# Performance work log

Measured on AMD Instinct MI355X. Metric: run time of the kernel, lower is better.

## Reference

```python
import jax, jax.numpy as jnp
import numpy as np

N_USERS = 100000
N_ITEMS = 50000
DIM = 64
N_EDGES = 4_000_000
NUM_LAYERS = 3


def setup_inputs() -> dict:
    key = jax.random.key(0)
    k1, k2, k3 = jax.random.split(key, 3)
    # xavier_uniform-like scale for embeddings
    scale = float(np.sqrt(6.0 / (N_USERS + DIM)))
    user_emb = jax.random.uniform(k1, (N_USERS, DIM), jnp.float32, -scale, scale)
    scale_i = float(np.sqrt(6.0 / (N_ITEMS + DIM)))
    item_emb = jax.random.uniform(k2, (N_ITEMS, DIM), jnp.float32, -scale_i, scale_i)
    edge_index = jax.random.randint(k3, (2, N_EDGES), 0, N_USERS + N_ITEMS, dtype=jnp.int64)
    return {"user_emb": user_emb, "item_emb": item_emb, "edge_index": edge_index}


def reference(user_emb, item_emb, edge_index):
    """LightGCN_W.encode_window: K rounds of symmetric-normalized SpMM, then layer mean."""
    n_users = user_emb.shape[0]
    n_nodes = n_users + item_emb.shape[0]
    row, col = edge_index[0], edge_index[1]  # messages flow row (source) -> col (target)

    # gcn_norm with add_self_loops=False (PyG LGConv default)
    ones = jnp.ones(row.shape[0], dtype=user_emb.dtype)
    deg = jax.ops.segment_sum(ones, col, num_segments=n_nodes)
    dinv = jnp.where(deg > 0, jax.lax.rsqrt(jnp.maximum(deg, 1e-12)), 0.0)
    norm = (dinv[row] * dinv[col])[:, None]  # [E, 1]

    x = jnp.concatenate([user_emb, item_emb], axis=0)  # [N, D]
    acc = x
    for _ in range(NUM_LAYERS):
        x = jax.ops.segment_sum(norm * x[row], col, num_segments=n_nodes)
        acc = acc + x
    out = acc / (NUM_LAYERS + 1)
    return out[:n_users], out[n_users:]
```

## Files before the change

### kernel.cpp

```cpp
#include <hip/hip_runtime.h>
#include <hip/hip_fp16.h>

#define DIM 64
#define BSH 8
#define BMASK 255u
#define NBMAX 1024
#define BINC 16384


__global__ void zero_ints(int* __restrict__ p, int n) {
    int i = blockIdx.x * blockDim.x + threadIdx.x;
    if (i < n) p[i] = 0;
}

__global__ __launch_bounds__(1024) void bucket_count_kernel(const int* __restrict__ edge, int E,
                                                            int* __restrict__ bcnt, int NB) {
    __shared__ int lcnt[NBMAX];
    for (int i = threadIdx.x; i < NB; i += 1024) lcnt[i] = 0;
    __syncthreads();
    int stride = gridDim.x * 1024;
    for (int i = blockIdx.x * 1024 + threadIdx.x; i < E; i += stride)
        atomicAdd(&lcnt[edge[E + i] >> BSH], 1);
    __syncthreads();
    for (int i = threadIdx.x; i < NB; i += 1024) {
        int v = lcnt[i];
        if (v) atomicAdd(&bcnt[i], v);
    }
}

__global__ __launch_bounds__(1024) void scan_kernel(const int* __restrict__ cnt,
                                                    int* __restrict__ offsets,
                                                    int* __restrict__ cursor,
                                                    int n) {
    __shared__ int lds[1024];
    const int T = 1024, K = 4, CHUNK = T * K;
    int carry = 0;
    for (int base = 0; base < n; base += CHUNK) {
        int v[K];
        int idx0 = base + (int)threadIdx.x * K;
#pragma unroll
        for (int k = 0; k < K; ++k) {
            int i = idx0 + k;
            v[k] = (i < n) ? cnt[i] : 0;
        }
        int tsum = v[0] + v[1] + v[2] + v[3];
        lds[threadIdx.x] = tsum;
        __syncthreads();
        int incl = tsum;
        for (int off = 1; off < T; off <<= 1) {
            int t = (threadIdx.x >= (unsigned)off) ? lds[threadIdx.x - off] : 0;
            __syncthreads();
            incl += t;
            lds[threadIdx.x] = incl;
            __syncthreads();
        }
        int total = lds[T - 1];
        int run = carry + (incl - tsum);
#pragma unroll
        for (int k = 0; k < K; ++k) {
            int i = idx0 + k;
            if (i < n) { offsets[i] = run; cursor[i] = run; }
            run += v[k];
        }
        carry += total;
        __syncthreads();
    }
    if (threadIdx.x == 0) offsets[n] = carry;
}

__global__ __launch_bounds__(1024) void bin_kernel(const int* __restrict__ edge, int E,
                                                   int* __restrict__ bcur,
                                                   unsigned* __restrict__ bin, int NB) {
    __shared__ unsigned stage[BINC];
    __shared__ int lcnt[NBMAX];
    __shared__ int lsc[NBMAX];
    __shared__ int lcur[NBMAX];
    __shared__ int gb[NBMAX];
    const int tid = (int)threadIdx.x;
    const int beg = (int)blockIdx.x * BINC;
    const int n = min(BINC, E - beg);

    lcnt[tid] = 0;
    __syncthreads();
    for (int i = tid; i < n; i += 1024)
        atomicAdd(&lcnt[edge[E + beg + i] >> BSH], 1);
    __syncthreads();
    lsc[tid] = lcnt[tid];
    __syncthreads();
    for (int off = 1; off < 1024; off <<= 1) {
        int t = (tid >= off) ? lsc[tid - off] : 0;
        __syncthreads();
        lsc[tid] += t;
        __syncthreads();
    }
    {
        int cb = lcnt[tid];
        lcur[tid] = lsc[tid] - cb;
        if (tid < NB) gb[tid] = cb ? atomicAdd(&bcur[tid], cb) : 0;
    }
    __syncthreads();
    for (int i = tid; i < n; i += 1024) {
        int r = edge[beg + i];
        int c = edge[E + beg + i];
        int b = c >> BSH;
        int slot = atomicAdd(&lcur[b], 1);
        stage[slot] = ((unsigned)r << BSH) | ((unsigned)c & BMASK);
    }
    __syncthreads();
    const int wid = tid >> 6, lane = tid & 63;
    for (int b = wid; b < NB; b += 16) {
        int cb = lcnt[b];
        if (!cb) continue;
        int lb = lsc[b] - cb;
        int g = gb[b];
        for (int l = lane; l < cb; l += 64)
            bin[g + l] = stage[lb + l];
    }
}

__global__ __launch_bounds__(256) void csr_kernel(const unsigned* __restrict__ bin,
                                                  const int* __restrict__ boff,
                                                  const float* __restrict__ user,
                                                  const float* __restrict__ item,
                                                  int nU,
                                                  int* __restrict__ offsets,
                                                  float* __restrict__ dinv,
                                                  float* __restrict__ rdinv,
                                                  int* __restrict__ row_sorted,
                                                  __half* __restrict__ y0,
                                                  int nN) {
    __shared__ int lcnt[256];
    __shared__ int lsc[256];
    __shared__ int lcur[256];
    __shared__ float sdinv[256];
    const int tid = (int)threadIdx.x;
    const int b = (int)blockIdx.x;
    const int beg = boff[b], end = boff[b + 1];
    lcnt[tid] = 0;
    __syncthreads();
    for (int i = beg + tid; i < end; i += 256)
        atomicAdd(&lcnt[bin[i] & BMASK], 1);
    __syncthreads();
    lsc[tid] = lcnt[tid];
    __syncthreads();
    for (int off = 1; off < 256; off <<= 1) {
        int t = (tid >= off) ? lsc[tid - off] : 0;
        __syncthreads();
        lsc[tid] += t;
        __syncthreads();
    }
    int cb = lcnt[tid];
    int lb = lsc[tid] - cb;
    lcur[tid] = lb;
    float dv = cb ? rsqrtf((float)cb) : 0.0f;
    sdinv[tid] = dv;
    int node = (b << BSH) + tid;
    if (node < nN) {
        offsets[node] = beg + lb;
        dinv[node] = dv;
        rdinv[node] = cb ? sqrtf((float)cb) : 0.0f;
        if (node == nN - 1) offsets[nN] = beg + lsc[tid];
    }
    __syncthreads();
    for (int i = beg + tid; i < end; i += 256) {
        unsigned e = bin[i];
        int c = (int)(e & BMASK);
        int p = atomicAdd(&lcur[c], 1);
        row_sorted[beg + p] = (int)(e >> BSH);
    }
    const int baseNode = b << BSH;
#pragma unroll
    for (int it = 0; it < 8; ++it) {
        int idx = it * 256 + tid;
        int ln = idx >> 3;
        int node2 = baseNode + ln;
        if (node2 < nN) {
            int qc = idx & 7;
            const float* src = (node2 < nU) ? user + (size_t)node2 * DIM
                                            : item + (size_t)(node2 - nU) * DIM;
            float4 e0 = ((const float4*)src)[qc * 2];
            float4 e1 = ((const float4*)src)[qc * 2 + 1];
            float dvn = sdinv[ln];
            float4 pack;
            __half2* p = (__half2*)&pack;
            p[0] = __floats2half2_rn(dvn * e0.x, dvn * e0.y);
            p[1] = __floats2half2_rn(dvn * e0.z, dvn * e0.w);
            p[2] = __floats2half2_rn(dvn * e1.x, dvn * e1.y);
            p[3] = __floats2half2_rn(dvn * e1.z, dvn * e1.w);
            ((float4*)y0)[(size_t)baseNode * 8 + idx] = pack;
        }
    }
}

__global__ __launch_bounds__(256) void layer_kernel(const int* __restrict__ offsets,
                                                    const int* __restrict__ row_sorted,
                                                    const float* __restrict__ dinv,
                                                    const __half* __restrict__ y_in,
                                                    __half* __restrict__ y_out,
                                                    int nN) {
    int wave = (int)((blockIdx.x * blockDim.x + threadIdx.x) >> 6);
    int lane = (int)(threadIdx.x & 63);
    if (wave >= nN) return;
    const int beg = offsets[wave];
    const int end = offsets[wave + 1];
    const int g = lane >> 3;
    const int q = lane & 7;
    const float4* yv = (const float4*)y_in;
    float a0 = 0, a1 = 0, a2 = 0, a3 = 0, a4 = 0, a5 = 0, a6 = 0, a7 = 0;
    const int last = end - 1;
    for (int base = beg; base < end; base += 16) {
        int e0 = base + g;
        int e1 = e0 + 8;
        int i0 = (e0 <= last) ? e0 : last;
        int i1 = (e1 <= last) ? e1 : last;
        float m0 = (e0 <= last) ? 1.0f : 0.0f;
        float m1 = (e1 <= last) ? 1.0f : 0.0f;
        int r0 = row_sorted[i0];
        int r1 = row_sorted[i1];
        float4 v0 = yv[(size_t)r0 * 8 + q];
        float4 v1 = yv[(size_t)r1 * 8 + q];
        const __half2* h0 = (const __half2*)&v0;
        const __half2* h1 = (const __half2*)&v1;
        float2 t;
        t = __half22float2(h0[0]); a0 = fmaf(m0, t.x, a0); a1 = fmaf(m0, t.y, a1);
        t = __half22float2(h0[1]); a2 = fmaf(m0, t.x, a2); a3 = fmaf(m0, t.y, a3);
        t = __half22float2(h0[2]); a4 = fmaf(m0, t.x, a4); a5 = fmaf(m0, t.y, a5);
        t = __half22float2(h0[3]); a6 = fmaf(m0, t.x, a6); a7 = fmaf(m0, t.y, a7);
        t = __half22float2(h1[0]); a0 = fmaf(m1, t.x, a0); a1 = fmaf(m1, t.y, a1);
        t = __half22float2(h1[1]); a2 = fmaf(m1, t.x, a2); a3 = fmaf(m1, t.y, a3);
        t = __half22float2(h1[2]); a4 = fmaf(m1, t.x, a4); a5 = fmaf(m1, t.y, a5);
        t = __half22float2(h1[3]); a6 = fmaf(m1, t.x, a6); a7 = fmaf(m1, t.y, a7);
    }
#pragma unroll
    for (int ofs = 8; ofs <= 32; ofs <<= 1) {
        a0 += __shfl_xor(a0, ofs);
        a1 += __shfl_xor(a1, ofs);
        a2 += __shfl_xor(a2, ofs);
        a3 += __shfl_xor(a3, ofs);
        a4 += __shfl_xor(a4, ofs);
        a5 += __shfl_xor(a5, ofs);
        a6 += __shfl_xor(a6, ofs);
        a7 += __shfl_xor(a7, ofs);
    }
    if (g == 0) {
        float dc = dinv[wave];
        float s = dc * dc;
        float4 pack;
        __half2* p = (__half2*)&pack;
        p[0] = __floats2half2_rn(s * a0, s * a1);
        p[1] = __floats2half2_rn(s * a2, s * a3);
        p[2] = __floats2half2_rn(s * a4, s * a5);
        p[3] = __floats2half2_rn(s * a6, s * a7);
        ((float4*)y_out)[(size_t)wave * 8 + q] = pack;
    }
}

__global__ __launch_bounds__(256) void final_kernel(const float* __restrict__ user,
                                                    const float* __restrict__ item,
                                                    const float* __restrict__ rdinv,
                                                    const __half* __restrict__ y1,
                                                    const __half* __restrict__ y2,
                                                    const __half* __restrict__ y3,
                                                    float* __restrict__ out,
                                                    int nU, int nN) {
    int c = blockIdx.x * blockDim.x + threadIdx.x;
    if (c >= nN * 8) return;
    int node = c >> 3;
    int qc = c & 7;
    float rd = 0.25f * rdinv[node];
    float4 h1 = ((const float4*)y1)[c];
    float4 h2 = ((const float4*)y2)[c];
    float4 h3 = ((const float4*)y3)[c];
    const float* src = (node < nU) ? user + (size_t)node * DIM
                                   : item + (size_t)(node - nU) * DIM;
    float4 e0 = ((const float4*)src)[qc * 2];
    float4 e1 = ((const float4*)src)[qc * 2 + 1];
    const __half2* p1 = (const __half2*)&h1;
    const __half2* p2 = (const __half2*)&h2;
    const __half2* p3 = (const __half2*)&h3;
    float r[8];
#pragma unroll
    for (int j = 0; j < 4; ++j) {
        float2 u1 = __half22float2(p1[j]);
        float2 u2 = __half22float2(p2[j]);
        float2 u3 = __half22float2(p3[j]);
        r[2 * j]     = u1.x + u2.x + u3.x;
        r[2 * j + 1] = u1.y + u2.y + u3.y;
    }
    float4 o0, o1;
    o0.x = 0.25f * e0.x + rd * r[0];
    o0.y = 0.25f * e0.y + rd * r[1];
    o0.z = 0.25f * e0.z + rd * r[2];
    o0.w = 0.25f * e0.w + rd * r[3];
    o1.x = 0.25f * e1.x + rd * r[4];
    o1.y = 0.25f * e1.y + rd * r[5];
    o1.z = 0.25f * e1.z + rd * r[6];
    o1.w = 0.25f * e1.w + rd * r[7];
    ((float4*)out)[(size_t)c * 2]     = o0;
    ((float4*)out)[(size_t)c * 2 + 1] = o1;
}


extern "C" void kernel_launch(void* const* d_in, const int* in_sizes, int n_in,
                              void* d_out, int out_size, void* d_ws, size_t ws_size,
                              hipStream_t stream) {
    const float* user = (const float*)d_in[0];
    const float* item = (const float*)d_in[1];
    const int*   edge = (const int*)d_in[2];

    const int nU = in_sizes[0] / DIM;
    const int nI = in_sizes[1] / DIM;
    const int nN = nU + nI;
    const int E  = in_sizes[2] / 2;
    const int total = nN * DIM;
    const int NB = (nN + 255) / 256;

    float* out = (float*)d_out;

    char* ws = (char*)d_ws;
    size_t off = 0;
    auto take = [&](size_t bytes) -> char* {
        char* p = ws + off;
        off = (off + bytes + 255) & ~(size_t)255;
        return p;
    };
    const size_t ybytes = (size_t)total * 2;
    const size_t binbytes = (size_t)E * 4;
    int*      bcnt       = (int*)  take((size_t)NB * 4);
    int*      boff       = (int*)  take((size_t)(NB + 1) * 4);
    int*      bcur       = (int*)  take((size_t)NB * 4);
    int*      offsets    = (int*)  take((size_t)(nN + 1) * 4);
    float*    dinv       = (float*)take((size_t)nN * 4);
    float*    rdinv      = (float*)take((size_t)nN * 4);
    int*      row_sorted = (int*)  take((size_t)E * 4);
    char*     regionA    = take(binbytes > ybytes ? binbytes : ybytes);
    char*     regionB    = take(ybytes);
    char*     regionC    = take(ybytes);
    unsigned* bin = (unsigned*)regionA;
    __half*   y1  = (__half*)regionA;
    __half*   y0  = (__half*)regionB;
    __half*   y3  = (__half*)regionB;
    __half*   y2  = (__half*)regionC;
    (void)ws_size; (void)n_in; (void)out_size;

    const int B = 256;
    dim3 blk(B);

    zero_ints<<<dim3((NB + B - 1) / B), blk, 0, stream>>>(bcnt, NB);
    bucket_count_kernel<<<dim3(256), dim3(1024), 0, stream>>>(edge, E, bcnt, NB);
    scan_kernel<<<dim3(1), dim3(1024), 0, stream>>>(bcnt, boff, bcur, NB);
    bin_kernel<<<dim3((E + BINC - 1) / BINC), dim3(1024), 0, stream>>>(edge, E, bcur, bin, NB);
    csr_kernel<<<dim3(NB), blk, 0, stream>>>(bin, boff, user, item, nU,
                                             offsets, dinv, rdinv, row_sorted, y0, nN);

    dim3 lgrid((nN + 3) / 4);
    layer_kernel<<<lgrid, blk, 0, stream>>>(offsets, row_sorted, dinv, y0, y1, nN);
    layer_kernel<<<lgrid, blk, 0, stream>>>(offsets, row_sorted, dinv, y1, y2, nN);
    layer_kernel<<<lgrid, blk, 0, stream>>>(offsets, row_sorted, dinv, y2, y3, nN);

    final_kernel<<<dim3((nN * 8 + B - 1) / B), blk, 0, stream>>>(user, item, rdinv,
                                                                 y1, y2, y3, out, nU, nN);
}
```

Measured before the change: 319.2 us.

## Split fp16 feature matrix into two 32-column halves and run per-half layer passes

```diff
diff --git a/kernel.cpp b/kernel.cpp
--- a/kernel.cpp
+++ b/kernel.cpp
@@ -2,10 +2,13 @@
 #include <hip/hip_fp16.h>
 
 #define DIM 64
+#define HDIM 32
 #define BSH 8
 #define BMASK 255u
 #define NBMAX 1024
 #define BINC 16384
+
+typedef __attribute__((ext_vector_type(4))) float f32x4;
 
 
 __global__ void zero_ints(int* __restrict__ p, int n) {
@@ -127,7 +130,8 @@
                                                   float* __restrict__ dinv,
                                                   float* __restrict__ rdinv,
                                                   int* __restrict__ row_sorted,
-                                                  __half* __restrict__ y0,
+                                                  __half* __restrict__ y0A,
+                                                  __half* __restrict__ y0B,
                                                   int nN) {
     __shared__ int lcnt[256];
     __shared__ int lsc[256];
@@ -187,38 +191,41 @@
             p[1] = __floats2half2_rn(dvn * e0.z, dvn * e0.w);
             p[2] = __floats2half2_rn(dvn * e1.x, dvn * e1.y);
             p[3] = __floats2half2_rn(dvn * e1.z, dvn * e1.w);
-            ((float4*)y0)[(size_t)baseNode * 8 + idx] = pack;
+            float4* dst = (qc < 4)
+                ? (float4*)y0A + (size_t)node2 * 4 + qc
+                : (float4*)y0B + (size_t)node2 * 4 + (qc - 4);
+            *dst = pack;
         }
     }
 }
 
-__global__ __launch_bounds__(256) void layer_kernel(const int* __restrict__ offsets,
-                                                    const int* __restrict__ row_sorted,
-                                                    const float* __restrict__ dinv,
-                                                    const __half* __restrict__ y_in,
-                                                    __half* __restrict__ y_out,
-                                                    int nN) {
+__global__ __launch_bounds__(256) void layer_pass_kernel(const int* __restrict__ offsets,
+                                                         const int* __restrict__ row_sorted,
+                                                         const float* __restrict__ dinv,
+                                                         const __half* __restrict__ y_in,
+                                                         __half* __restrict__ y_out,
+                                                         int nN) {
     int wave = (int)((blockIdx.x * blockDim.x + threadIdx.x) >> 6);
     int lane = (int)(threadIdx.x & 63);
     if (wave >= nN) return;
     const int beg = offsets[wave];
     const int end = offsets[wave + 1];
-    const int g = lane >> 3;
-    const int q = lane & 7;
+    const int g = lane >> 2;
+    const int q = lane & 3;
     const float4* yv = (const float4*)y_in;
     float a0 = 0, a1 = 0, a2 = 0, a3 = 0, a4 = 0, a5 = 0, a6 = 0, a7 = 0;
     const int last = end - 1;
-    for (int base = beg; base < end; base += 16) {
+    for (int base = beg; base < end; base += 32) {
         int e0 = base + g;
-        int e1 = e0 + 8;
+        int e1 = e0 + 16;
         int i0 = (e0 <= last) ? e0 : last;
         int i1 = (e1 <= last) ? e1 : last;
         float m0 = (e0 <= last) ? 1.0f : 0.0f;
         float m1 = (e1 <= last) ? 1.0f : 0.0f;
-        int r0 = row_sorted[i0];
-        int r1 = row_sorted[i1];
-        float4 v0 = yv[(size_t)r0 * 8 + q];
-        float4 v1 = yv[(size_t)r1 * 8 + q];
+        int r0 = __builtin_nontemporal_load(row_sorted + i0);
+        int r1 = __builtin_nontemporal_load(row_sorted + i1);
+        float4 v0 = yv[(size_t)r0 * 4 + q];
+        float4 v1 = yv[(size_t)r1 * 4 + q];
         const __half2* h0 = (const __half2*)&v0;
         const __half2* h1 = (const __half2*)&v1;
         float2 t;
@@ -232,7 +239,7 @@
         t = __half22float2(h1[3]); a6 = fmaf(m1, t.x, a6); a7 = fmaf(m1, t.y, a7);
     }
 #pragma unroll
-    for (int ofs = 8; ofs <= 32; ofs <<= 1) {
+    for (int ofs = 4; ofs <= 32; ofs <<= 1) {
         a0 += __shfl_xor(a0, ofs);
         a1 += __shfl_xor(a1, ofs);
         a2 += __shfl_xor(a2, ofs);
@@ -245,22 +252,26 @@
     if (g == 0) {
         float dc = dinv[wave];
         float s = dc * dc;
-        float4 pack;
-        __half2* p = (__half2*)&pack;
-        p[0] = __floats2half2_rn(s * a0, s * a1);
-        p[1] = __floats2half2_rn(s * a2, s * a3);
-        p[2] = __floats2half2_rn(s * a4, s * a5);
-        p[3] = __floats2half2_rn(s * a6, s * a7);
-        ((float4*)y_out)[(size_t)wave * 8 + q] = pack;
+        f32x4 pack;
+        __half2 ph[4];
+        ph[0] = __floats2half2_rn(s * a0, s * a1);
+        ph[1] = __floats2half2_rn(s * a2, s * a3);
+        ph[2] = __floats2half2_rn(s * a4, s * a5);
+        ph[3] = __floats2half2_rn(s * a6, s * a7);
+        pack = *(const f32x4*)ph;
+        __builtin_nontemporal_store(pack, (f32x4*)y_out + (size_t)wave * 4 + q);
     }
 }
 
 __global__ __launch_bounds__(256) void final_kernel(const float* __restrict__ user,
                                                     const float* __restrict__ item,
                                                     const float* __restrict__ rdinv,
-                                                    const __half* __restrict__ y1,
-                                                    const __half* __restrict__ y2,
-                                                    const __half* __restrict__ y3,
+                                                    const __half* __restrict__ y1A,
+                                                    const __half* __restrict__ y1B,
+                                                    const __half* __restrict__ y2A,
+                                                    const __half* __restrict__ y2B,
+                                                    const __half* __restrict__ y3A,
+                                                    const __half* __restrict__ y3B,
                                                     float* __restrict__ out,
                                                     int nU, int nN) {
     int c = blockIdx.x * blockDim.x + threadIdx.x;
@@ -268,9 +279,13 @@
     int node = c >> 3;
     int qc = c & 7;
     float rd = 0.25f * rdinv[node];
-    float4 h1 = ((const float4*)y1)[c];
-    float4 h2 = ((const float4*)y2)[c];
-    float4 h3 = ((const float4*)y3)[c];
+    size_t hidx = (size_t)node * 4 + (qc & 3);
+    const __half* t1 = (qc < 4) ? y1A : y1B;
+    const __half* t2 = (qc < 4) ? y2A : y2B;
+    const __half* t3 = (qc < 4) ? y3A : y3B;
+    float4 h1 = ((const float4*)t1)[hidx];
+    float4 h2 = ((const float4*)t2)[hidx];
+    float4 h3 = ((const float4*)t3)[hidx];
     const float* src = (node < nU) ? user + (size_t)node * DIM
                                    : item + (size_t)(node - nU) * DIM;
     float4 e0 = ((const float4*)src)[qc * 2];
@@ -312,7 +327,6 @@
     const int nI = in_sizes[1] / DIM;
     const int nN = nU + nI;
     const int E  = in_sizes[2] / 2;
-    const int total = nN * DIM;
     const int NB = (nN + 255) / 256;
 
     float* out = (float*)d_out;
@@ -324,7 +338,7 @@
         off = (off + bytes + 255) & ~(size_t)255;
         return p;
     };
-    const size_t ybytes = (size_t)total * 2;
+    const size_t hbytes = (size_t)nN * HDIM * 2;
     const size_t binbytes = (size_t)E * 4;
     int*      bcnt       = (int*)  take((size_t)NB * 4);
     int*      boff       = (int*)  take((size_t)(NB + 1) * 4);
@@ -333,14 +347,18 @@
     float*    dinv       = (float*)take((size_t)nN * 4);
     float*    rdinv      = (float*)take((size_t)nN * 4);
     int*      row_sorted = (int*)  take((size_t)E * 4);
-    char*     regionA    = take(binbytes > ybytes ? binbytes : ybytes);
-    char*     regionB    = take(ybytes);
-    char*     regionC    = take(ybytes);
-    unsigned* bin = (unsigned*)regionA;
-    __half*   y1  = (__half*)regionA;
-    __half*   y0  = (__half*)regionB;
-    __half*   y3  = (__half*)regionB;
-    __half*   y2  = (__half*)regionC;
+    char*     R1 = take(binbytes > 2 * hbytes ? binbytes : 2 * hbytes);
+    char*     R2 = take(2 * hbytes);
+    char*     R3 = take(2 * hbytes);
+    unsigned* bin = (unsigned*)R1;
+    __half*   y1A = (__half*)R1;
+    __half*   y1B = (__half*)(R1 + hbytes);
+    __half*   y0A = (__half*)R2;
+    __half*   y0B = (__half*)(R2 + hbytes);
+    __half*   y3A = y0A;
+    __half*   y3B = y0B;
+    __half*   y2A = (__half*)R3;
+    __half*   y2B = (__half*)(R3 + hbytes);
     (void)ws_size; (void)n_in; (void)out_size;
 
     const int B = 256;
@@ -351,13 +369,17 @@
     scan_kernel<<<dim3(1), dim3(1024), 0, stream>>>(bcnt, boff, bcur, NB);
     bin_kernel<<<dim3((E + BINC - 1) / BINC), dim3(1024), 0, stream>>>(edge, E, bcur, bin, NB);
     csr_kernel<<<dim3(NB), blk, 0, stream>>>(bin, boff, user, item, nU,
-                                             offsets, dinv, rdinv, row_sorted, y0, nN);
+                                             offsets, dinv, rdinv, row_sorted, y0A, y0B, nN);
 
     dim3 lgrid((nN + 3) / 4);
-    layer_kernel<<<lgrid, blk, 0, stream>>>(offsets, row_sorted, dinv, y0, y1, nN);
-    layer_kernel<<<lgrid, blk, 0, stream>>>(offsets, row_sorted, dinv, y1, y2, nN);
-    layer_kernel<<<lgrid, blk, 0, stream>>>(offsets, row_sorted, dinv, y2, y3, nN);
+    layer_pass_kernel<<<lgrid, blk, 0, stream>>>(offsets, row_sorted, dinv, y0A, y1A, nN);
+    layer_pass_kernel<<<lgrid, blk, 0, stream>>>(offsets, row_sorted, dinv, y0B, y1B, nN);
+    layer_pass_kernel<<<lgrid, blk, 0, stream>>>(offsets, row_sorted, dinv, y1A, y2A, nN);
+    layer_pass_kernel<<<lgrid, blk, 0, stream>>>(offsets, row_sorted, dinv, y1B, y2B, nN);
+    layer_pass_kernel<<<lgrid, blk, 0, stream>>>(offsets, row_sorted, dinv, y2A, y3A, nN);
+    layer_pass_kernel<<<lgrid, blk, 0, stream>>>(offsets, row_sorted, dinv, y2B, y3B, nN);
 
     final_kernel<<<dim3((nN * 8 + B - 1) / B), blk, 0, stream>>>(user, item, rdinv,
-                                                                 y1, y2, y3, out, nU, nN);
-}
+                                                                 y1A, y1B, y2A, y2B, y3A, y3B,
+                                                                 out, nU, nN);
+}
```

Result: slower. 478.3 us (+49.8%).

## Pad CSR rows to multiples of 16 with sentinel zero row to drop masking

Applied to the files above, without the earlier changes.

```diff
diff --git a/kernel.cpp b/kernel.cpp
--- a/kernel.cpp
+++ b/kernel.cpp
@@ -6,6 +6,9 @@
 #define BMASK 255u
 #define NBMAX 1024
 #define BINC 16384
+#define PADSTRIDE 4096
+
+typedef __attribute__((ext_vector_type(4))) float f32x4;
 
 
 __global__ void zero_ints(int* __restrict__ p, int n) {
@@ -123,15 +126,17 @@
                                                   const float* __restrict__ user,
                                                   const float* __restrict__ item,
                                                   int nU,
-                                                  int* __restrict__ offsets,
+                                                  int* __restrict__ poff,
+                                                  int* __restrict__ pcnt,
                                                   float* __restrict__ dinv,
                                                   float* __restrict__ rdinv,
-                                                  int* __restrict__ row_sorted,
+                                                  int* __restrict__ row_padded,
                                                   __half* __restrict__ y0,
                                                   int nN) {
     __shared__ int lcnt[256];
-    __shared__ int lsc[256];
+    __shared__ int lps[256];
     __shared__ int lcur[256];
+    __shared__ int spbeg[256];
     __shared__ float sdinv[256];
     const int tid = (int)threadIdx.x;
     const int b = (int)blockIdx.x;
@@ -141,33 +146,38 @@
     for (int i = beg + tid; i < end; i += 256)
         atomicAdd(&lcnt[bin[i] & BMASK], 1);
     __syncthreads();
-    lsc[tid] = lcnt[tid];
+    const int cb = lcnt[tid];
+    const int pc = (cb + 15) & ~15;
+    lps[tid] = pc;
     __syncthreads();
     for (int off = 1; off < 256; off <<= 1) {
-        int t = (tid >= off) ? lsc[tid - off] : 0;
-        __syncthreads();
-        lsc[tid] += t;
-        __syncthreads();
-    }
-    int cb = lcnt[tid];
-    int lb = lsc[tid] - cb;
-    lcur[tid] = lb;
+        int t = (tid >= off) ? lps[tid - off] : 0;
+        __syncthreads();
+        lps[tid] += t;
+        __syncthreads();
+    }
+    const int pbase = beg + b * PADSTRIDE;
+    const int pbeg = pbase + (lps[tid] - pc);
+    spbeg[tid] = pbeg;
+    lcur[tid] = pbeg;
     float dv = cb ? rsqrtf((float)cb) : 0.0f;
     sdinv[tid] = dv;
     int node = (b << BSH) + tid;
     if (node < nN) {
-        offsets[node] = beg + lb;
+        poff[node] = pbeg;
+        pcnt[node] = pc;
         dinv[node] = dv;
         rdinv[node] = cb ? sqrtf((float)cb) : 0.0f;
-        if (node == nN - 1) offsets[nN] = beg + lsc[tid];
     }
     __syncthreads();
     for (int i = beg + tid; i < end; i += 256) {
         unsigned e = bin[i];
         int c = (int)(e & BMASK);
         int p = atomicAdd(&lcur[c], 1);
-        row_sorted[beg + p] = (int)(e >> BSH);
-    }
+        row_padded[p] = (int)(e >> BSH);
+    }
+    for (int k = cb; k < pc; ++k)
+        row_padded[spbeg[tid] + k] = nN;
     const int baseNode = b << BSH;
 #pragma unroll
     for (int it = 0; it < 8; ++it) {
@@ -192,44 +202,48 @@
     }
 }
 
-__global__ __launch_bounds__(256) void layer_kernel(const int* __restrict__ offsets,
-                                                    const int* __restrict__ row_sorted,
+__global__ void zero_row_kernel(__half* __restrict__ r1, __half* __restrict__ r2,
+                                __half* __restrict__ r3, int nN) {
+    int t = threadIdx.x;
+    size_t o = (size_t)nN * DIM + t;
+    r1[o] = __float2half(0.0f);
+    r2[o] = __float2half(0.0f);
+    r3[o] = __float2half(0.0f);
+}
+
+__global__ __launch_bounds__(256) void layer_kernel(const int* __restrict__ poff,
+                                                    const int* __restrict__ pcnt,
                                                     const float* __restrict__ dinv,
+                                                    const int* __restrict__ row_padded,
                                                     const __half* __restrict__ y_in,
                                                     __half* __restrict__ y_out,
                                                     int nN) {
     int wave = (int)((blockIdx.x * blockDim.x + threadIdx.x) >> 6);
     int lane = (int)(threadIdx.x & 63);
     if (wave >= nN) return;
-    const int beg = offsets[wave];
-    const int end = offsets[wave + 1];
+    const int beg = poff[wave];
+    const int n = pcnt[wave];
     const int g = lane >> 3;
     const int q = lane & 7;
     const float4* yv = (const float4*)y_in;
     float a0 = 0, a1 = 0, a2 = 0, a3 = 0, a4 = 0, a5 = 0, a6 = 0, a7 = 0;
-    const int last = end - 1;
-    for (int base = beg; base < end; base += 16) {
-        int e0 = base + g;
-        int e1 = e0 + 8;
-        int i0 = (e0 <= last) ? e0 : last;
-        int i1 = (e1 <= last) ? e1 : last;
-        float m0 = (e0 <= last) ? 1.0f : 0.0f;
-        float m1 = (e1 <= last) ? 1.0f : 0.0f;
-        int r0 = row_sorted[i0];
-        int r1 = row_sorted[i1];
+    for (int base = 0; base < n; base += 16) {
+        int e0 = beg + base + g;
+        int r0 = __builtin_nontemporal_load(row_padded + e0);
+        int r1 = __builtin_nontemporal_load(row_padded + e0 + 8);
         float4 v0 = yv[(size_t)r0 * 8 + q];
         float4 v1 = yv[(size_t)r1 * 8 + q];
         const __half2* h0 = (const __half2*)&v0;
         const __half2* h1 = (const __half2*)&v1;
         float2 t;
-        t = __half22float2(h0[0]); a0 = fmaf(m0, t.x, a0); a1 = fmaf(m0, t.y, a1);
-        t = __half22float2(h0[1]); a2 = fmaf(m0, t.x, a2); a3 = fmaf(m0, t.y, a3);
-        t = __half22float2(h0[2]); a4 = fmaf(m0, t.x, a4); a5 = fmaf(m0, t.y, a5);
-        t = __half22float2(h0[3]); a6 = fmaf(m0, t.x, a6); a7 = fmaf(m0, t.y, a7);
-        t = __half22float2(h1[0]); a0 = fmaf(m1, t.x, a0); a1 = fmaf(m1, t.y, a1);
-        t = __half22float2(h1[1]); a2 = fmaf(m1, t.x, a2); a3 = fmaf(m1, t.y, a3);
-        t = __half22float2(h1[2]); a4 = fmaf(m1, t.x, a4); a5 = fmaf(m1, t.y, a5);
-        t = __half22float2(h1[3]); a6 = fmaf(m1, t.x, a6); a7 = fmaf(m1, t.y, a7);
+        t = __half22float2(h0[0]); a0 += t.x; a1 += t.y;
+        t = __half22float2(h0[1]); a2 += t.x; a3 += t.y;
+        t = __half22float2(h0[2]); a4 += t.x; a5 += t.y;
+        t = __half22float2(h0[3]); a6 += t.x; a7 += t.y;
+        t = __half22float2(h1[0]); a0 += t.x; a1 += t.y;
+        t = __half22float2(h1[1]); a2 += t.x; a3 += t.y;
+        t = __half22float2(h1[2]); a4 += t.x; a5 += t.y;
+        t = __half22float2(h1[3]); a6 += t.x; a7 += t.y;
     }
 #pragma unroll
     for (int ofs = 8; ofs <= 32; ofs <<= 1) {
@@ -245,13 +259,13 @@
     if (g == 0) {
         float dc = dinv[wave];
         float s = dc * dc;
-        float4 pack;
-        __half2* p = (__half2*)&pack;
-        p[0] = __floats2half2_rn(s * a0, s * a1);
-        p[1] = __floats2half2_rn(s * a2, s * a3);
-        p[2] = __floats2half2_rn(s * a4, s * a5);
-        p[3] = __floats2half2_rn(s * a6, s * a7);
-        ((float4*)y_out)[(size_t)wave * 8 + q] = pack;
+        __half2 ph[4];
+        ph[0] = __floats2half2_rn(s * a0, s * a1);
+        ph[1] = __floats2half2_rn(s * a2, s * a3);
+        ph[2] = __floats2half2_rn(s * a4, s * a5);
+        ph[3] = __floats2half2_rn(s * a6, s * a7);
+        f32x4 pack = *(const f32x4*)ph;
+        __builtin_nontemporal_store(pack, (f32x4*)y_out + (size_t)wave * 8 + q);
     }
 }
 
@@ -312,7 +326,6 @@
     const int nI = in_sizes[1] / DIM;
     const int nN = nU + nI;
     const int E  = in_sizes[2] / 2;
-    const int total = nN * DIM;
     const int NB = (nN + 255) / 256;
 
     float* out = (float*)d_out;
@@ -324,23 +337,25 @@
         off = (off + bytes + 255) & ~(size_t)255;
         return p;
     };
-    const size_t ybytes = (size_t)total * 2;
+    const size_t ytab = (size_t)(nN + 1) * DIM * 2;
     const size_t binbytes = (size_t)E * 4;
+    const size_t padbytes = ((size_t)E + (size_t)NB * PADSTRIDE) * 4;
     int*      bcnt       = (int*)  take((size_t)NB * 4);
     int*      boff       = (int*)  take((size_t)(NB + 1) * 4);
     int*      bcur       = (int*)  take((size_t)NB * 4);
-    int*      offsets    = (int*)  take((size_t)(nN + 1) * 4);
+    int*      poff       = (int*)  take((size_t)nN * 4);
+    int*      pcnt       = (int*)  take((size_t)nN * 4);
     float*    dinv       = (float*)take((size_t)nN * 4);
     float*    rdinv      = (float*)take((size_t)nN * 4);
-    int*      row_sorted = (int*)  take((size_t)E * 4);
-    char*     regionA    = take(binbytes > ybytes ? binbytes : ybytes);
-    char*     regionB    = take(ybytes);
-    char*     regionC    = take(ybytes);
-    unsigned* bin = (unsigned*)regionA;
-    __half*   y1  = (__half*)regionA;
-    __half*   y0  = (__half*)regionB;
-    __half*   y3  = (__half*)regionB;
-    __half*   y2  = (__half*)regionC;
+    int*      row_padded = (int*)  take(padbytes);
+    char*     R1 = take(binbytes > ytab ? binbytes : ytab);
+    char*     R2 = take(ytab);
+    char*     R3 = take(ytab);
+    unsigned* bin = (unsigned*)R1;
+    __half*   y1  = (__half*)R1;
+    __half*   y0  = (__half*)R2;
+    __half*   y3  = (__half*)R2;
+    __half*   y2  = (__half*)R3;
     (void)ws_size; (void)n_in; (void)out_size;
 
     const int B = 256;
@@ -351,12 +366,13 @@
     scan_kernel<<<dim3(1), dim3(1024), 0, stream>>>(bcnt, boff, bcur, NB);
     bin_kernel<<<dim3((E + BINC - 1) / BINC), dim3(1024), 0, stream>>>(edge, E, bcur, bin, NB);
     csr_kernel<<<dim3(NB), blk, 0, stream>>>(bin, boff, user, item, nU,
-                                             offsets, dinv, rdinv, row_sorted, y0, nN);
+                                             poff, pcnt, dinv, rdinv, row_padded, y0, nN);
+    zero_row_kernel<<<dim3(1), dim3(64), 0, stream>>>(y1, y0, y2, nN);
 
     dim3 lgrid((nN + 3) / 4);
-    layer_kernel<<<lgrid, blk, 0, stream>>>(offsets, row_sorted, dinv, y0, y1, nN);
-    layer_kernel<<<lgrid, blk, 0, stream>>>(offsets, row_sorted, dinv, y1, y2, nN);
-    layer_kernel<<<lgrid, blk, 0, stream>>>(offsets, row_sorted, dinv, y2, y3, nN);
+    layer_kernel<<<lgrid, blk, 0, stream>>>(poff, pcnt, dinv, row_padded, y0, y1, nN);
+    layer_kernel<<<lgrid, blk, 0, stream>>>(poff, pcnt, dinv, row_padded, y1, y2, nN);
+    layer_kernel<<<lgrid, blk, 0, stream>>>(poff, pcnt, dinv, row_padded, y2, y3, nN);
 
     final_kernel<<<dim3((nN * 8 + B - 1) / B), blk, 0, stream>>>(user, item, rdinv,
                                                                  y1, y2, y3, out, nU, nN);
```

New measurement: 368.5 us. 15.4% more time.

## Replace bucket count/scan with fixed-stride arenas and fuse final combine into last layer

Applied to the files above, without the earlier changes.

```diff
diff --git a/kernel.cpp b/kernel.cpp
--- a/kernel.cpp
+++ b/kernel.cpp
@@ -6,66 +6,14 @@
 #define BMASK 255u
 #define NBMAX 1024
 #define BINC 16384
+#define BSTRIDE 8192
+
+typedef __attribute__((ext_vector_type(4))) float f32x4;
 
 
 __global__ void zero_ints(int* __restrict__ p, int n) {
     int i = blockIdx.x * blockDim.x + threadIdx.x;
     if (i < n) p[i] = 0;
-}
-
-__global__ __launch_bounds__(1024) void bucket_count_kernel(const int* __restrict__ edge, int E,
-                                                            int* __restrict__ bcnt, int NB) {
-    __shared__ int lcnt[NBMAX];
-    for (int i = threadIdx.x; i < NB; i += 1024) lcnt[i] = 0;
-    __syncthreads();
-    int stride = gridDim.x * 1024;
-    for (int i = blockIdx.x * 1024 + threadIdx.x; i < E; i += stride)
-        atomicAdd(&lcnt[edge[E + i] >> BSH], 1);
-    __syncthreads();
-    for (int i = threadIdx.x; i < NB; i += 1024) {
-        int v = lcnt[i];
-        if (v) atomicAdd(&bcnt[i], v);
-    }
-}
-
-__global__ __launch_bounds__(1024) void scan_kernel(const int* __restrict__ cnt,
-                                                    int* __restrict__ offsets,
-                                                    int* __restrict__ cursor,
-                                                    int n) {
-    __shared__ int lds[1024];
-    const int T = 1024, K = 4, CHUNK = T * K;
-    int carry = 0;
-    for (int base = 0; base < n; base += CHUNK) {
-        int v[K];
-        int idx0 = base + (int)threadIdx.x * K;
-#pragma unroll
-        for (int k = 0; k < K; ++k) {
-            int i = idx0 + k;
-            v[k] = (i < n) ? cnt[i] : 0;
-        }
-        int tsum = v[0] + v[1] + v[2] + v[3];
-        lds[threadIdx.x] = tsum;
-        __syncthreads();
-        int incl = tsum;
-        for (int off = 1; off < T; off <<= 1) {
-            int t = (threadIdx.x >= (unsigned)off) ? lds[threadIdx.x - off] : 0;
-            __syncthreads();
-            incl += t;
-            lds[threadIdx.x] = incl;
-            __syncthreads();
-        }
-        int total = lds[T - 1];
-        int run = carry + (incl - tsum);
-#pragma unroll
-        for (int k = 0; k < K; ++k) {
-            int i = idx0 + k;
-            if (i < n) { offsets[i] = run; cursor[i] = run; }
-            run += v[k];
-        }
-        carry += total;
-        __syncthreads();
-    }
-    if (threadIdx.x == 0) offsets[n] = carry;
 }
 
 __global__ __launch_bounds__(1024) void bin_kernel(const int* __restrict__ edge, int E,
@@ -112,18 +60,19 @@
         int cb = lcnt[b];
         if (!cb) continue;
         int lb = lsc[b] - cb;
-        int g = gb[b];
+        int g = b * BSTRIDE + gb[b];
         for (int l = lane; l < cb; l += 64)
             bin[g + l] = stage[lb + l];
     }
 }
 
 __global__ __launch_bounds__(256) void csr_kernel(const unsigned* __restrict__ bin,
-                                                  const int* __restrict__ boff,
+                                                  const int* __restrict__ bcnt,
                                                   const float* __restrict__ user,
                                                   const float* __restrict__ item,
                                                   int nU,
-                                                  int* __restrict__ offsets,
+                                                  int* __restrict__ poff,
+                                                  int* __restrict__ pdeg,
                                                   float* __restrict__ dinv,
                                                   float* __restrict__ rdinv,
                                                   int* __restrict__ row_sorted,
@@ -135,11 +84,12 @@
     __shared__ float sdinv[256];
     const int tid = (int)threadIdx.x;
     const int b = (int)blockIdx.x;
-    const int beg = boff[b], end = boff[b + 1];
+    const int abase = b * BSTRIDE;
+    const int cnt = bcnt[b];
     lcnt[tid] = 0;
     __syncthreads();
-    for (int i = beg + tid; i < end; i += 256)
-        atomicAdd(&lcnt[bin[i] & BMASK], 1);
+    for (int i = tid; i < cnt; i += 256)
+        atomicAdd(&lcnt[bin[abase + i] & BMASK], 1);
     __syncthreads();
     lsc[tid] = lcnt[tid];
     __syncthreads();
@@ -149,24 +99,24 @@
         lsc[tid] += t;
         __syncthreads();
     }
-    int cb = lcnt[tid];
-    int lb = lsc[tid] - cb;
-    lcur[tid] = lb;
+    const int cb = lcnt[tid];
+    const int lb = lsc[tid] - cb;
+    lcur[tid] = abase + lb;
     float dv = cb ? rsqrtf((float)cb) : 0.0f;
     sdinv[tid] = dv;
     int node = (b << BSH) + tid;
     if (node < nN) {
-        offsets[node] = beg + lb;
+        poff[node] = abase + lb;
+        pdeg[node] = cb;
         dinv[node] = dv;
         rdinv[node] = cb ? sqrtf((float)cb) : 0.0f;
-        if (node == nN - 1) offsets[nN] = beg + lsc[tid];
-    }
-    __syncthreads();
-    for (int i = beg + tid; i < end; i += 256) {
-        unsigned e = bin[i];
+    }
+    __syncthreads();
+    for (int i = tid; i < cnt; i += 256) {
+        unsigned e = bin[abase + i];
         int c = (int)(e & BMASK);
         int p = atomicAdd(&lcur[c], 1);
-        row_sorted[beg + p] = (int)(e >> BSH);
+        row_sorted[p] = (int)(e >> BSH);
     }
     const int baseNode = b << BSH;
 #pragma unroll
@@ -192,17 +142,24 @@
     }
 }
 
-__global__ __launch_bounds__(256) void layer_kernel(const int* __restrict__ offsets,
+template<bool LAST>
+__global__ __launch_bounds__(256) void layer_kernel(const int* __restrict__ poff,
+                                                    const int* __restrict__ pdeg,
+                                                    const float* __restrict__ dinv,
                                                     const int* __restrict__ row_sorted,
-                                                    const float* __restrict__ dinv,
                                                     const __half* __restrict__ y_in,
                                                     __half* __restrict__ y_out,
-                                                    int nN) {
+                                                    const float* __restrict__ user,
+                                                    const float* __restrict__ item,
+                                                    const float* __restrict__ rdinv,
+                                                    const __half* __restrict__ y_prev,
+                                                    float* __restrict__ out,
+                                                    int nU, int nN) {
     int wave = (int)((blockIdx.x * blockDim.x + threadIdx.x) >> 6);
     int lane = (int)(threadIdx.x & 63);
     if (wave >= nN) return;
-    const int beg = offsets[wave];
-    const int end = offsets[wave + 1];
+    const int beg = poff[wave];
+    const int end = beg + pdeg[wave];
     const int g = lane >> 3;
     const int q = lane & 7;
     const float4* yv = (const float4*)y_in;
@@ -215,8 +172,8 @@
         int i1 = (e1 <= last) ? e1 : last;
         float m0 = (e0 <= last) ? 1.0f : 0.0f;
         float m1 = (e1 <= last) ? 1.0f : 0.0f;
-        int r0 = row_sorted[i0];
-        int r1 = row_sorted[i1];
+        int r0 = __builtin_nontemporal_load(row_sorted + i0);
+        int r1 = __builtin_nontemporal_load(row_sorted + i1);
         float4 v0 = yv[(size_t)r0 * 8 + q];
         float4 v1 = yv[(size_t)r1 * 8 + q];
         const __half2* h0 = (const __half2*)&v0;
@@ -244,60 +201,47 @@
     }
     if (g == 0) {
         float dc = dinv[wave];
-        float s = dc * dc;
-        float4 pack;
-        __half2* p = (__half2*)&pack;
-        p[0] = __floats2half2_rn(s * a0, s * a1);
-        p[1] = __floats2half2_rn(s * a2, s * a3);
-        p[2] = __floats2half2_rn(s * a4, s * a5);
-        p[3] = __floats2half2_rn(s * a6, s * a7);
-        ((float4*)y_out)[(size_t)wave * 8 + q] = pack;
-    }
-}
-
-__global__ __launch_bounds__(256) void final_kernel(const float* __restrict__ user,
-                                                    const float* __restrict__ item,
-                                                    const float* __restrict__ rdinv,
-                                                    const __half* __restrict__ y1,
-                                                    const __half* __restrict__ y2,
-                                                    const __half* __restrict__ y3,
-                                                    float* __restrict__ out,
-                                                    int nU, int nN) {
-    int c = blockIdx.x * blockDim.x + threadIdx.x;
-    if (c >= nN * 8) return;
-    int node = c >> 3;
-    int qc = c & 7;
-    float rd = 0.25f * rdinv[node];
-    float4 h1 = ((const float4*)y1)[c];
-    float4 h2 = ((const float4*)y2)[c];
-    float4 h3 = ((const float4*)y3)[c];
-    const float* src = (node < nU) ? user + (size_t)node * DIM
-                                   : item + (size_t)(node - nU) * DIM;
-    float4 e0 = ((const float4*)src)[qc * 2];
-    float4 e1 = ((const float4*)src)[qc * 2 + 1];
-    const __half2* p1 = (const __half2*)&h1;
-    const __half2* p2 = (const __half2*)&h2;
-    const __half2* p3 = (const __half2*)&h3;
-    float r[8];
+        if (!LAST) {
+            float s = dc * dc;
+            __half2 ph[4];
+            ph[0] = __floats2half2_rn(s * a0, s * a1);
+            ph[1] = __floats2half2_rn(s * a2, s * a3);
+            ph[2] = __floats2half2_rn(s * a4, s * a5);
+            ph[3] = __floats2half2_rn(s * a6, s * a7);
+            f32x4 pack = *(const f32x4*)ph;
+            __builtin_nontemporal_store(pack, (f32x4*)y_out + (size_t)wave * 8 + q);
+        } else {
+            float rd = rdinv[wave];
+            float4 y1r = ((const float4*)y_prev)[(size_t)wave * 8 + q];
+            float4 y2r = ((const float4*)y_in)[(size_t)wave * 8 + q];
+            const __half2* p1 = (const __half2*)&y1r;
+            const __half2* p2 = (const __half2*)&y2r;
+            float w[8];
 #pragma unroll
-    for (int j = 0; j < 4; ++j) {
-        float2 u1 = __half22float2(p1[j]);
-        float2 u2 = __half22float2(p2[j]);
-        float2 u3 = __half22float2(p3[j]);
-        r[2 * j]     = u1.x + u2.x + u3.x;
-        r[2 * j + 1] = u1.y + u2.y + u3.y;
-    }
-    float4 o0, o1;
-    o0.x = 0.25f * e0.x + rd * r[0];
-    o0.y = 0.25f * e0.y + rd * r[1];
-    o0.z = 0.25f * e0.z + rd * r[2];
-    o0.w = 0.25f * e0.w + rd * r[3];
-    o1.x = 0.25f * e1.x + rd * r[4];
-    o1.y = 0.25f * e1.y + rd * r[5];
-    o1.z = 0.25f * e1.z + rd * r[6];
-    o1.w = 0.25f * e1.w + rd * r[7];
-    ((float4*)out)[(size_t)c * 2]     = o0;
-    ((float4*)out)[(size_t)c * 2 + 1] = o1;
+            for (int j = 0; j < 4; ++j) {
+                float2 u1 = __half22float2(p1[j]);
+                float2 u2 = __half22float2(p2[j]);
+                w[2 * j]     = u1.x + u2.x;
+                w[2 * j + 1] = u1.y + u2.y;
+            }
+            const float* src = (wave < nU) ? user + (size_t)wave * DIM
+                                           : item + (size_t)(wave - nU) * DIM;
+            float4 e0 = ((const float4*)src)[q * 2];
+            float4 e1 = ((const float4*)src)[q * 2 + 1];
+            float4 o0, o1;
+            o0.x = 0.25f * (e0.x + rd * w[0] + dc * a0);
+            o0.y = 0.25f * (e0.y + rd * w[1] + dc * a1);
+            o0.z = 0.25f * (e0.z + rd * w[2] + dc * a2);
+            o0.w = 0.25f * (e0.w + rd * w[3] + dc * a3);
+            o1.x = 0.25f * (e1.x + rd * w[4] + dc * a4);
+            o1.y = 0.25f * (e1.y + rd * w[5] + dc * a5);
+            o1.z = 0.25f * (e1.z + rd * w[6] + dc * a6);
+            o1.w = 0.25f * (e1.w + rd * w[7] + dc * a7);
+            float4* o4 = (float4*)(out + (size_t)wave * DIM + q * 8);
+            o4[0] = o0;
+            o4[1] = o1;
+        }
+    }
 }
 
 
@@ -312,7 +256,6 @@
     const int nI = in_sizes[1] / DIM;
     const int nN = nU + nI;
     const int E  = in_sizes[2] / 2;
-    const int total = nN * DIM;
     const int NB = (nN + 255) / 256;
 
     float* out = (float*)d_out;
@@ -324,40 +267,39 @@
         off = (off + bytes + 255) & ~(size_t)255;
         return p;
     };
-    const size_t ybytes = (size_t)total * 2;
-    const size_t binbytes = (size_t)E * 4;
-    int*      bcnt       = (int*)  take((size_t)NB * 4);
-    int*      boff       = (int*)  take((size_t)(NB + 1) * 4);
+    const size_t ytab = (size_t)nN * DIM * 2;
+    const size_t arena = (size_t)NB * BSTRIDE * 4;
     int*      bcur       = (int*)  take((size_t)NB * 4);
-    int*      offsets    = (int*)  take((size_t)(nN + 1) * 4);
+    int*      poff       = (int*)  take((size_t)nN * 4);
+    int*      pdeg       = (int*)  take((size_t)nN * 4);
     float*    dinv       = (float*)take((size_t)nN * 4);
     float*    rdinv      = (float*)take((size_t)nN * 4);
-    int*      row_sorted = (int*)  take((size_t)E * 4);
-    char*     regionA    = take(binbytes > ybytes ? binbytes : ybytes);
-    char*     regionB    = take(ybytes);
-    char*     regionC    = take(ybytes);
-    unsigned* bin = (unsigned*)regionA;
-    __half*   y1  = (__half*)regionA;
-    __half*   y0  = (__half*)regionB;
-    __half*   y3  = (__half*)regionB;
-    __half*   y2  = (__half*)regionC;
+    int*      row_sorted = (int*)  take(arena);
+    char*     R1 = take(arena > ytab ? arena : ytab);
+    char*     R2 = take(ytab);
+    char*     R3 = take(ytab);
+    unsigned* bin = (unsigned*)R1;
+    __half*   y1  = (__half*)R1;
+    __half*   y0  = (__half*)R2;
+    __half*   y2  = (__half*)R3;
     (void)ws_size; (void)n_in; (void)out_size;
 
     const int B = 256;
     dim3 blk(B);
 
-    zero_ints<<<dim3((NB + B - 1) / B), blk, 0, stream>>>(bcnt, NB);
-    bucket_count_kernel<<<dim3(256), dim3(1024), 0, stream>>>(edge, E, bcnt, NB);
-    scan_kernel<<<dim3(1), dim3(1024), 0, stream>>>(bcnt, boff, bcur, NB);
+    zero_ints<<<dim3((NB + B - 1) / B), blk, 0, stream>>>(bcur, NB);
     bin_kernel<<<dim3((E + BINC - 1) / BINC), dim3(1024), 0, stream>>>(edge, E, bcur, bin, NB);
-    csr_kernel<<<dim3(NB), blk, 0, stream>>>(bin, boff, user, item, nU,
-                                             offsets, dinv, rdinv, row_sorted, y0, nN);
+    csr_kernel<<<dim3(NB), blk, 0, stream>>>(bin, bcur, user, item, nU,
+                                             poff, pdeg, dinv, rdinv, row_sorted, y0, nN);
 
     dim3 lgrid((nN + 3) / 4);
-    layer_kernel<<<lgrid, blk, 0, stream>>>(offsets, row_sorted, dinv, y0, y1, nN);
-    layer_kernel<<<lgrid, blk, 0, stream>>>(offsets, row_sorted, dinv, y1, y2, nN);
-    layer_kernel<<<lgrid, blk, 0, stream>>>(offsets, row_sorted, dinv, y2, y3, nN);
-
-    final_kernel<<<dim3((nN * 8 + B - 1) / B), blk, 0, stream>>>(user, item, rdinv,
-                                                                 y1, y2, y3, out, nU, nN);
-}
+    layer_kernel<false><<<lgrid, blk, 0, stream>>>(poff, pdeg, dinv, row_sorted, y0, y1,
+                                                   nullptr, nullptr, nullptr, nullptr, nullptr,
+                                                   nU, nN);
+    layer_kernel<false><<<lgrid, blk, 0, stream>>>(poff, pdeg, dinv, row_sorted, y1, y2,
+                                                   nullptr, nullptr, nullptr, nullptr, nullptr,
+                                                   nU, nN);
+    layer_kernel<true ><<<lgrid, blk, 0, stream>>>(poff, pdeg, dinv, row_sorted, y2, nullptr,
+                                                   user, item, rdinv, y1, out,
+                                                   nU, nN);
+}
```

New measurement: 341.1 us. 6.9% more time.
